# Optimization experiments

Hardware: AMD Instinct MI355X
Metric: run time of the kernel (lower is better)

Reference implementation:

```python
import jax, jax.numpy as jnp
import numpy as np

D = 4096          # input_dims
P = 1             # p in Get_Atten_map_mc
NUM_IMG = 16
N_PER = 64        # objects per image
R_PER = 512       # relations per image
LN_EPS = 1e-5


def _linear_params(key, out_dim, in_dim):
    kw, kb = jax.random.split(key)
    w = jax.random.normal(kw, (out_dim, in_dim), jnp.float32) * 0.02
    b = jax.random.normal(kb, (out_dim,), jnp.float32) * 0.02
    return w, b


def setup_inputs() -> dict:
    key = jax.random.key(0)
    ks = jax.random.split(key, 12)
    N = NUM_IMG * N_PER
    R = NUM_IMG * R_PER

    obj_feats = jax.random.normal(ks[0], (N, D), jnp.float32)
    phr_feats = jax.random.normal(ks[1], (R, D), jnp.float32)

    # im_inds: uniform N_PER objects per image
    im_inds = jnp.repeat(jnp.arange(NUM_IMG, dtype=jnp.int64), N_PER)

    # rel_inds: [img_idx, subj_global, obj_global], R_PER rels per image,
    # subject/object indices local-to-image then offset to global ids.
    subj_loc = jax.random.randint(ks[2], (NUM_IMG, R_PER), 0, N_PER)
    obj_loc = jax.random.randint(ks[3], (NUM_IMG, R_PER), 0, N_PER)
    offs = (jnp.arange(NUM_IMG) * N_PER)[:, None]
    img_col = jnp.repeat(jnp.arange(NUM_IMG), R_PER)
    rel_inds = jnp.stack(
        [img_col, (subj_loc + offs).reshape(-1), (obj_loc + offs).reshape(-1)], axis=1
    ).astype(jnp.int64)

    Ws_w, Ws_b = _linear_params(ks[4], D, D)       # ws
    Wo_w, Wo_b = _linear_params(ks[5], D, D)       # wo
    Ww_w, Ww_b = _linear_params(ks[6], P, D)       # w (attention logits)
    Wc_w, Wc_b = _linear_params(ks[7], D // 2, D)  # conv Linear
    Wt1_w, Wt1_b = _linear_params(ks[8], D // 4, D)
    Wt2_w, Wt2_b = _linear_params(ks[9], D, D // 4)
    ln_g = jnp.ones((D // 4,), jnp.float32)
    ln_b = jnp.zeros((D // 4,), jnp.float32)

    return {
        "obj_feats": obj_feats, "phr_feats": phr_feats,
        "im_inds": im_inds, "rel_inds": rel_inds, "num_img": NUM_IMG,
        "Ws_w": Ws_w, "Ws_b": Ws_b, "Wo_w": Wo_w, "Wo_b": Wo_b,
        "Ww_w": Ww_w, "Ww_b": Ww_b, "Wc_w": Wc_w, "Wc_b": Wc_b,
        "Wt1_w": Wt1_w, "Wt1_b": Wt1_b, "ln_g": ln_g, "ln_b": ln_b,
        "Wt2_w": Wt2_w, "Wt2_b": Wt2_b,
    }


def reference(obj_feats, phr_feats, im_inds, rel_inds, num_img,
              Ws_w, Ws_b, Wo_w, Wo_b, Ww_w, Ww_b, Wc_w, Wc_b,
              Wt1_w, Wt1_b, ln_g, ln_b, Wt2_w, Wt2_b):
    N, d = obj_feats.shape
    n_per = N // num_img
    R = rel_inds.shape[0]
    r_per = R // num_img
    p = Ww_w.shape[0]

    # ws/wo projections over all objects (original recomputes them per image
    # on the full obj_feats -- identical math, computed once here).
    ws_all = obj_feats @ Ws_w.T + Ws_b
    wo_all = obj_feats @ Wo_w.T + Wo_b

    subj = rel_inds[:, 1]
    objc = rel_inds[:, 2]
    prod = ws_all[subj] * wo_all[objc]               # [R, D]
    atten_f = (prod * phr_feats) @ Ww_w.T + Ww_b     # [R, p]

    # conv on object features
    conv_all = jax.nn.relu(obj_feats @ Wc_w.T + Wc_b)  # [N, D/2]

    subj_i = subj.reshape(num_img, r_per)
    objc_i = objc.reshape(num_img, r_per)
    af_i = atten_f.reshape(num_img, r_per, p)
    conv_i = conv_all.reshape(num_img, n_per, -1)

    self_mask = 1.0 - jnp.eye(n_per, dtype=jnp.float32)[:, :, None]  # [n,n,1]

    def per_image(s, o, af, conv_feats):
        head = jnp.minimum(s.min(), o.min())
        A = jnp.zeros((n_per, n_per, p), jnp.float32).at[s - head, o - head].add(af)
        A = jax.nn.sigmoid(A) * self_mask
        A = A / A.sum(1)                               # [n,n,p] / [n,p] (col-normalize)
        A2 = jnp.concatenate([A, A.transpose(1, 0, 2)], axis=-1)  # [n,n,2p]
        # mc_matmul: concat of per-channel mm -> channel-major reshape
        return jnp.einsum('ijc,jd->icd', A2, conv_feats).reshape(n_per, -1)

    ctx = jax.vmap(per_image)(subj_i, objc_i, af_i, conv_i)  # [num_img, n, 2p*D/2]
    ctx = ctx.reshape(N, -1)                                  # [N, D]

    # trans: Linear -> LayerNorm -> ReLU -> Linear
    h = ctx @ Wt1_w.T + Wt1_b
    mu = h.mean(-1, keepdims=True)
    var = ((h - mu) ** 2).mean(-1, keepdims=True)
    h = (h - mu) * jax.lax.rsqrt(var + LN_EPS) * ln_g + ln_b
    h = jax.nn.relu(h)
    out = h @ Wt2_w.T + Wt2_b

    return jax.nn.relu(obj_feats + out)
```

## Files before the change

### kernel.cpp

```cpp
#include <hip/hip_runtime.h>
#include <hip/hip_bf16.h>
#include <math.h>

#define D_   4096
#define NIMG 16
#define NPER 64
#define RPER 512
#define NTOT 1024
#define RTOT 8192
#define DC   2048
#define DT   1024
#define LDA  8192

typedef __attribute__((ext_vector_type(4))) float f32x4;
typedef __attribute__((ext_vector_type(8))) short bf16x8;

#define GLD16(gp, lp) __builtin_amdgcn_global_load_lds( \
    (const __attribute__((address_space(1))) unsigned int*)(gp), \
    (__attribute__((address_space(3))) unsigned int*)(lp), 16, 0, 0)

template<int N> __device__ __forceinline__ void waitvm() {
    asm volatile("s_waitcnt vmcnt(%0)" :: "n"(N) : "memory");
}

__device__ __forceinline__ void fma4(float4& d, float s, const float4 c) {
    d.x = fmaf(s, c.x, d.x); d.y = fmaf(s, c.y, d.y);
    d.z = fmaf(s, c.z, d.z); d.w = fmaf(s, c.w, d.w);
}
__device__ __forceinline__ void st4bf(__hip_bfloat16* p, float4 v) {
    union { __hip_bfloat16 h[4]; ushort4 u; } cv;
    cv.h[0] = __float2bfloat16(v.x); cv.h[1] = __float2bfloat16(v.y);
    cv.h[2] = __float2bfloat16(v.z); cv.h[3] = __float2bfloat16(v.w);
    *(ushort4*)p = cv.u;
}

__global__ __launch_bounds__(256) void cast_all(
    const float* __restrict__ obj, __hip_bfloat16* __restrict__ obj_bf,
    const float* __restrict__ Ws, const float* __restrict__ Wo,
    const float* __restrict__ Wc, __hip_bfloat16* __restrict__ wbuf,
    const float* __restrict__ b0, const float* __restrict__ b1,
    const float* __restrict__ b2, float* __restrict__ cb)
{
    const int b = blockIdx.x;
    if (b < 22528) {
        const float* s; __hip_bfloat16* d; int rb;
        if (b < 2048)       { s = obj; d = obj_bf;          rb = b; }
        else if (b < 10240) { s = Ws;  d = wbuf;            rb = b - 2048; }
        else if (b < 18432) { s = Wo;  d = wbuf + 16777216; rb = b - 10240; }
        else                { s = Wc;  d = wbuf + 33554432; rb = b - 18432; }
        const int i = (rb * 256 + threadIdx.x) * 8;
        float4 v0 = *(const float4*)(s + i);
        float4 v1 = *(const float4*)(s + i + 4);
        union { __hip_bfloat16 h[8]; ushort4 u[2]; } cv;
        cv.h[0] = __float2bfloat16(v0.x); cv.h[1] = __float2bfloat16(v0.y);
        cv.h[2] = __float2bfloat16(v0.z); cv.h[3] = __float2bfloat16(v0.w);
        cv.h[4] = __float2bfloat16(v1.x); cv.h[5] = __float2bfloat16(v1.y);
        cv.h[6] = __float2bfloat16(v1.z); cv.h[7] = __float2bfloat16(v1.w);
        *(ushort4*)(d + i)     = cv.u[0];
        *(ushort4*)(d + i + 4) = cv.u[1];
    } else {
        const int i = (b - 22528) * 256 + threadIdx.x;
        float v;
        if (i < 4096) v = b0[i];
        else if (i < 8192) v = b1[i - 4096];
        else v = b2[i - 8192];
        cb[i] = v;
    }
}

__global__ __launch_bounds__(256) void cast2(
    const float* __restrict__ Wt1, const float* __restrict__ Wt2,
    __hip_bfloat16* __restrict__ wt1r, __hip_bfloat16* __restrict__ wt2b)
{
    const int b = blockIdx.x;
    const int t = threadIdx.x;
    const float* s; __hip_bfloat16* d;
    if (b < 2048) {
        const int r = b, c = t * 8;
        s = Wt1 + (size_t)(r & 1023) * 4096 + (r >> 10) * 2048 + c;
        d = wt1r + (size_t)r * 2048 + c;
    } else {
        const int i = ((b - 2048) * 256 + t) * 8;
        s = Wt2 + i;
        d = wt2b + i;
    }
    float4 v0 = *(const float4*)s;
    float4 v1 = *(const float4*)(s + 4);
    union { __hip_bfloat16 h[8]; ushort4 u[2]; } cv;
    cv.h[0] = __float2bfloat16(v0.x); cv.h[1] = __float2bfloat16(v0.y);
    cv.h[2] = __float2bfloat16(v0.z); cv.h[3] = __float2bfloat16(v0.w);
    cv.h[4] = __float2bfloat16(v1.x); cv.h[5] = __float2bfloat16(v1.y);
    cv.h[6] = __float2bfloat16(v1.z); cv.h[7] = __float2bfloat16(v1.w);
    *(ushort4*)d       = cv.u[0];
    *(ushort4*)(d + 4) = cv.u[1];
}

template<int BM, int BN>
__global__ __launch_bounds__(256) void gemm_p2(
    const ushort* __restrict__ A, const ushort* __restrict__ B,
    const float* __restrict__ bias, const float* __restrict__ resid,
    float* __restrict__ C, __hip_bfloat16* __restrict__ C2,
    int M, int K, int ldc, int mode, int reluStart)
{
    constexpr int MREP = BM / 32;
    constexpr int NREP = BN / 32;
    constexpr int SLOTS = (BM + BN) * 4;
    constexpr int NPW = SLOTS / 256;
    constexpr int BUFE = SLOTS * 8;

    __shared__ ushort lds[3][BUFE];

    const int t = threadIdx.x;
    const int lane = t & 63;
    const int wid = t >> 6;
    const int wr = wid >> 1, wc = wid & 1;

    const int MT = M / BM;
    const int G = gridDim.x;
    const int bid = blockIdx.x;
    const int wgid = (bid & 7) * (G >> 3) + (bid >> 3);
    const int nt = wgid / MT, mt = wgid % MT;
    const int bm = mt * BM, bn = nt * BN;

    const ushort* gp[NPW];
    int loff[NPW];
#pragma unroll
    for (int i = 0; i < NPW; ++i) {
        const int slot = i * 256 + t;
        const bool isA = slot < BM * 4;
        const int s2 = isA ? slot : slot - BM * 4;
        const int row = s2 >> 2;
        const int q = (s2 & 3) ^ ((row >> 1) & 3);
        gp[i] = (isA ? A + (size_t)(bm + row) * K : B + (size_t)(bn + row) * K) + q * 8;
        loff[i] = slot * 8;
    }

    auto stage = [&](int b, int kpos) {
#pragma unroll
        for (int i = 0; i < NPW; ++i) GLD16(gp[i] + kpos, &lds[b][loff[i]]);
    };

    int aoff[MREP], boff[NREP];
    const int sx = (((lane >> 4) ^ ((lane >> 1) & 3))) << 3;
#pragma unroll
    for (int m = 0; m < MREP; ++m)
        aoff[m] = (wr * (BM / 2) + (lane & 15) + m * 16) * 32 + sx;
#pragma unroll
    for (int n = 0; n < NREP; ++n)
        boff[n] = BM * 32 + (wc * (BN / 2) + (lane & 15) + n * 16) * 32 + sx;

    f32x4 acc[MREP][NREP] = {};

    const int NT = K >> 5;
    stage(0, 0);
    stage(1, 32);
    if constexpr (NPW == 2) waitvm<2>();
    else if constexpr (NPW == 3) waitvm<3>();
    else waitvm<4>();
    __builtin_amdgcn_sched_barrier(0);
    __builtin_amdgcn_s_barrier();
    __builtin_amdgcn_sched_barrier(0);

    for (int tt = 0; tt < NT; ++tt) {
        const bool pf = (tt + 2 < NT);
        if (pf) stage((tt + 2) % 3, (tt + 2) << 5);
        __builtin_amdgcn_sched_barrier(0);

        const ushort* lb = lds[tt % 3];
        bf16x8 af[MREP], bfv[NREP];
#pragma unroll
        for (int m = 0; m < MREP; ++m) af[m] = *(const bf16x8*)(lb + aoff[m]);
#pragma unroll
        for (int n = 0; n < NREP; ++n) bfv[n] = *(const bf16x8*)(lb + boff[n]);
#pragma unroll
        for (int m = 0; m < MREP; ++m)
#pragma unroll
            for (int n = 0; n < NREP; ++n)
                acc[m][n] = __builtin_amdgcn_mfma_f32_16x16x32_bf16(
                    af[m], bfv[n], acc[m][n], 0, 0, 0);

        __builtin_amdgcn_sched_barrier(0);
        if (pf) {
            if constexpr (NPW == 2) waitvm<2>();
            else if constexpr (NPW == 3) waitvm<3>();
            else waitvm<4>();
        } else {
            waitvm<0>();
        }
        __builtin_amdgcn_sched_barrier(0);
        __builtin_amdgcn_s_barrier();
        __builtin_amdgcn_sched_barrier(0);
    }

    const int col0 = bn + wc * (BN / 2) + (lane & 15);
    const int row0 = bm + wr * (BM / 2) + ((lane >> 4) << 2);
#pragma unroll
    for (int m = 0; m < MREP; ++m) {
#pragma unroll
        for (int n = 0; n < NREP; ++n) {
            const int cn = col0 + n * 16;
            const float bz = bias ? bias[cn] : 0.f;
#pragma unroll
            for (int rg = 0; rg < 4; ++rg) {
                const int gm = row0 + m * 16 + rg;
                float v = acc[m][n][rg] + bz;
                if (mode == 2) {
                    v = fmaxf(v + resid[(size_t)gm * ldc + cn], 0.f);
                    C[(size_t)gm * ldc + cn] = v;
                } else if (mode == 4) {
                    if (cn < reluStart) {
                        C[(size_t)gm * ldc + cn] = v;
                    } else {
                        C2[(size_t)gm * 2048 + (cn - 8192)] =
                            __float2bfloat16(fmaxf(v, 0.f));
                    }
                } else {
                    C[(size_t)gm * ldc + cn] = v;
                }
            }
        }
    }
}

__global__ __launch_bounds__(256) void atten_kernel(
    const float* __restrict__ allout, const float* __restrict__ phr,
    const int* __restrict__ rel, const float* __restrict__ Www,
    const float* __restrict__ Wwb, float* __restrict__ atten)
{
    const int r = blockIdx.x;
    const int s = rel[r * 3 + 1], o = rel[r * 3 + 2];
    const int t = threadIdx.x;
    const float4* pws = (const float4*)(allout + (size_t)s * LDA);
    const float4* pwo = (const float4*)(allout + (size_t)o * LDA + 4096);
    const float4* pph = (const float4*)(phr + (size_t)r * D_);
    const float4* pww = (const float4*)Www;
    float sum = 0.f;
    for (int qq = t; qq < D_ / 4; qq += 256) {
        float4 a = pws[qq], b = pwo[qq], c = pph[qq], w = pww[qq];
        sum += a.x * b.x * c.x * w.x + a.y * b.y * c.y * w.y
             + a.z * b.z * c.z * w.z + a.w * b.w * c.w * w.w;
    }
    for (int off = 32; off > 0; off >>= 1) sum += __shfl_down(sum, off);
    __shared__ float red[4];
    if ((t & 63) == 0) red[t >> 6] = sum;
    __syncthreads();
    if (t == 0) atten[r] = red[0] + red[1] + red[2] + red[3] + Wwb[0];
}

__global__ __launch_bounds__(256) void build_A(
    const int* __restrict__ rel, const float* __restrict__ atten,
    float* __restrict__ Anorm)
{
    const int g = blockIdx.x;
    const int t = threadIdx.x;
    __shared__ float Am[64][64];
    __shared__ float S[64];
    __shared__ int headSh;
    for (int i = t; i < 4096; i += 256) ((float*)Am)[i] = 0.f;
    if (t == 0) headSh = 0x7fffffff;

    int lmin = 0x7fffffff;
    for (int rr = t; rr < RPER; rr += 256) {
        const int base = (g * RPER + rr) * 3;
        lmin = min(lmin, min(rel[base + 1], rel[base + 2]));
    }
    for (int off = 32; off > 0; off >>= 1) lmin = min(lmin, __shfl_down(lmin, off));
    __syncthreads();
    if ((t & 63) == 0) atomicMin(&headSh, lmin);
    __syncthreads();
    const int head = headSh;

    for (int rr = t; rr < RPER; rr += 256) {
        const int base = (g * RPER + rr) * 3;
        atomicAdd(&Am[rel[base + 1] - head][rel[base + 2] - head],
                  atten[g * RPER + rr]);
    }
    __syncthreads();

    for (int idx = t; idx < 4096; idx += 256) {
        const int i = idx >> 6, j = idx & 63;
        float v = 1.f / (1.f + expf(-Am[i][j]));
        if (i == j) v = 0.f;
        Am[i][j] = v;
    }
    __syncthreads();

    if (t < 64) {
        float sum = 0.f;
        for (int k = 0; k < 64; ++k) sum += Am[t][k];
        S[t] = sum;
    }
    __syncthreads();

    float* outg = Anorm + (size_t)g * 4096;
    for (int idx = t; idx < 4096; idx += 256) {
        const int j = idx & 63;
        outg[idx] = ((const float*)Am)[idx] / S[j];
    }
}

__global__ __launch_bounds__(256) void amult_ln(
    const float* __restrict__ Anorm, const float* __restrict__ P,
    const float* __restrict__ w1b, const float* __restrict__ gamma,
    const float* __restrict__ beta, __hip_bfloat16* __restrict__ hb)
{
    const int g = blockIdx.x >> 6;
    const int i = blockIdx.x & 63;
    const int t = threadIdx.x;
    __shared__ float Ar[64], Ac[64];
    if (t < 64) Ar[t] = Anorm[(size_t)g * 4096 + i * 64 + t];
    else if (t < 128) { const int j = t - 64; Ac[j] = Anorm[(size_t)g * 4096 + j * 64 + i]; }
    __syncthreads();

    const float* pg = P + (size_t)g * 64 * 2048;
    float4 v = {0, 0, 0, 0};
    for (int j = 0; j < 64; ++j) {
        float4 p1 = *(const float4*)(pg + (size_t)j * 2048 + (t << 2));
        float4 p2 = *(const float4*)(pg + (size_t)j * 2048 + 1024 + (t << 2));
        fma4(v, Ar[j], p1);
        fma4(v, Ac[j], p2);
    }
    float4 b0 = *(const float4*)(w1b + (t << 2));
    v.x += b0.x; v.y += b0.y; v.z += b0.z; v.w += b0.w;

    float s  = v.x + v.y + v.z + v.w;
    float ss = v.x * v.x + v.y * v.y + v.z * v.z + v.w * v.w;
    for (int off = 32; off > 0; off >>= 1) {
        s  += __shfl_down(s, off);
        ss += __shfl_down(ss, off);
    }
    __shared__ float rs[4], rss[4];
    if ((t & 63) == 0) { rs[t >> 6] = s; rss[t >> 6] = ss; }
    __syncthreads();
    const float tot  = rs[0] + rs[1] + rs[2] + rs[3];
    const float tot2 = rss[0] + rss[1] + rss[2] + rss[3];
    const float mu   = tot * (1.f / DT);
    const float var  = tot2 * (1.f / DT) - mu * mu;
    const float rstd = rsqrtf(var + 1e-5f);
    float4 g4 = *(const float4*)(gamma + (t << 2));
    float4 b4 = *(const float4*)(beta + (t << 2));
    float4 o;
    o.x = fmaxf(fmaf((v.x - mu) * rstd, g4.x, b4.x), 0.f);
    o.y = fmaxf(fmaf((v.y - mu) * rstd, g4.y, b4.y), 0.f);
    o.z = fmaxf(fmaf((v.z - mu) * rstd, g4.z, b4.z), 0.f);
    o.w = fmaxf(fmaf((v.w - mu) * rstd, g4.w, b4.w), 0.f);
    st4bf(hb + (size_t)(g * 64 + i) * DT + (t << 2), o);
}

extern "C" void kernel_launch(void* const* d_in, const int* in_sizes, int n_in,
                              void* d_out, int out_size, void* d_ws, size_t ws_size,
                              hipStream_t stream)
{
    const float* obj   = (const float*)d_in[0];
    const float* phr   = (const float*)d_in[1];
    const int*   rel   = (const int*)d_in[3];
    const float* Ws_w  = (const float*)d_in[5];
    const float* Ws_b  = (const float*)d_in[6];
    const float* Wo_w  = (const float*)d_in[7];
    const float* Wo_b  = (const float*)d_in[8];
    const float* Ww_w  = (const float*)d_in[9];
    const float* Ww_b  = (const float*)d_in[10];
    const float* Wc_w  = (const float*)d_in[11];
    const float* Wc_b  = (const float*)d_in[12];
    const float* Wt1_w = (const float*)d_in[13];
    const float* Wt1_b = (const float*)d_in[14];
    const float* ln_g  = (const float*)d_in[15];
    const float* ln_b  = (const float*)d_in[16];
    const float* Wt2_w = (const float*)d_in[17];
    const float* Wt2_b = (const float*)d_in[18];
    float* out = (float*)d_out;

    float* ws = (float*)d_ws;
    __hip_bfloat16* wbuf   = (__hip_bfloat16*)ws;
    __hip_bfloat16* wt1r   = (__hip_bfloat16*)ws;
    __hip_bfloat16* wt2b   = (__hip_bfloat16*)(ws + 2097152);
    __hip_bfloat16* obj_bf = (__hip_bfloat16*)(ws + 20971520);
    float* allout = ws + 23068672;
    float* Pbuf   = allout;
    __hip_bfloat16* h_bf = (__hip_bfloat16*)(allout + 2097152);
    __hip_bfloat16* conv_bf = (__hip_bfloat16*)(ws + 31457280);
    float* atten  = ws + 32505856;
    float* Anorm  = ws + 32514048;
    float* cbias  = ws + 32579584;

    const dim3 blk(256);

    cast_all<<<dim3(22568), blk, 0, stream>>>(
        obj, obj_bf, Ws_w, Wo_w, Wc_w, wbuf, Ws_b, Wo_b, Wc_b, cbias);

    gemm_p2<128, 128><<<dim3(640), blk, 0, stream>>>(
        (const ushort*)obj_bf, (const ushort*)wbuf, cbias, nullptr,
        allout, conv_bf, NTOT, D_, LDA, 4, 8192);

    cast2<<<dim3(4096), blk, 0, stream>>>(Wt1_w, Wt2_w, wt1r, wt2b);

    atten_kernel<<<dim3(RTOT), blk, 0, stream>>>(allout, phr, rel, Ww_w, Ww_b, atten);
    build_A<<<dim3(NIMG), blk, 0, stream>>>(rel, atten, Anorm);

    gemm_p2<64, 64><<<dim3(512), blk, 0, stream>>>(
        (const ushort*)conv_bf, (const ushort*)wt1r, nullptr, nullptr,
        Pbuf, nullptr, NTOT, DC, DC, 0, 0);

    amult_ln<<<dim3(1024), blk, 0, stream>>>(Anorm, Pbuf, Wt1_b, ln_g, ln_b, h_bf);

    gemm_p2<128, 128><<<dim3(256), blk, 0, stream>>>(
        (const ushort*)h_bf, (const ushort*)wt2b, Wt2_b, obj,
        out, nullptr, NTOT, DT, D_, 2, 0);
}
```

Measured before the change: 318.0 us.

## Store Ws/Wo projections as bf16, merge weight casts, retile final GEMM

The first GEMM now writes the Ws/Wo projection outputs as bf16 instead of fp32, and the attention kernel reads these bf16 rows with 16-byte loads, roughly halving the gather traffic. The Wt1/Wt2 cast kernel is folded into the main cast kernel so one launch handles every weight conversion, with the workspace layout rearranged so the buffers no longer alias. The final GEMM switches from 128x128 to 64x128 tiles with twice as many blocks for better occupancy. Storing the projections in bf16 loses precision in the attention logits.

```diff
diff --git a/kernel.cpp b/kernel.cpp
--- a/kernel.cpp
+++ b/kernel.cpp
@@ -10,7 +10,7 @@
 #define RTOT 8192
 #define DC   2048
 #define DT   1024
-#define LDA  8192
+#define LDW  8192
 
 typedef __attribute__((ext_vector_type(4))) float f32x4;
 typedef __attribute__((ext_vector_type(8))) short bf16x8;
@@ -33,66 +33,49 @@
     cv.h[2] = __float2bfloat16(v.z); cv.h[3] = __float2bfloat16(v.w);
     *(ushort4*)p = cv.u;
 }
+__device__ __forceinline__ float bf2f(ushort u) {
+    union { float f; unsigned int i; } c; c.i = (unsigned int)u << 16; return c.f;
+}
 
 __global__ __launch_bounds__(256) void cast_all(
     const float* __restrict__ obj, __hip_bfloat16* __restrict__ obj_bf,
     const float* __restrict__ Ws, const float* __restrict__ Wo,
     const float* __restrict__ Wc, __hip_bfloat16* __restrict__ wbuf,
+    const float* __restrict__ Wt1, __hip_bfloat16* __restrict__ wt1r,
+    const float* __restrict__ Wt2, __hip_bfloat16* __restrict__ wt2b,
     const float* __restrict__ b0, const float* __restrict__ b1,
     const float* __restrict__ b2, float* __restrict__ cb)
 {
     const int b = blockIdx.x;
-    if (b < 22528) {
-        const float* s; __hip_bfloat16* d; int rb;
-        if (b < 2048)       { s = obj; d = obj_bf;          rb = b; }
-        else if (b < 10240) { s = Ws;  d = wbuf;            rb = b - 2048; }
-        else if (b < 18432) { s = Wo;  d = wbuf + 16777216; rb = b - 10240; }
-        else                { s = Wc;  d = wbuf + 33554432; rb = b - 18432; }
-        const int i = (rb * 256 + threadIdx.x) * 8;
-        float4 v0 = *(const float4*)(s + i);
-        float4 v1 = *(const float4*)(s + i + 4);
-        union { __hip_bfloat16 h[8]; ushort4 u[2]; } cv;
-        cv.h[0] = __float2bfloat16(v0.x); cv.h[1] = __float2bfloat16(v0.y);
-        cv.h[2] = __float2bfloat16(v0.z); cv.h[3] = __float2bfloat16(v0.w);
-        cv.h[4] = __float2bfloat16(v1.x); cv.h[5] = __float2bfloat16(v1.y);
-        cv.h[6] = __float2bfloat16(v1.z); cv.h[7] = __float2bfloat16(v1.w);
-        *(ushort4*)(d + i)     = cv.u[0];
-        *(ushort4*)(d + i + 4) = cv.u[1];
-    } else {
-        const int i = (b - 22528) * 256 + threadIdx.x;
+    const int t = threadIdx.x;
+    if (b >= 26624) {
+        const int i = (b - 26624) * 256 + t;
         float v;
         if (i < 4096) v = b0[i];
         else if (i < 8192) v = b1[i - 4096];
         else v = b2[i - 8192];
         cb[i] = v;
-    }
-}
-
-__global__ __launch_bounds__(256) void cast2(
-    const float* __restrict__ Wt1, const float* __restrict__ Wt2,
-    __hip_bfloat16* __restrict__ wt1r, __hip_bfloat16* __restrict__ wt2b)
-{
-    const int b = blockIdx.x;
-    const int t = threadIdx.x;
+        return;
+    }
     const float* s; __hip_bfloat16* d;
-    if (b < 2048) {
-        const int r = b, c = t * 8;
-        s = Wt1 + (size_t)(r & 1023) * 4096 + (r >> 10) * 2048 + c;
-        d = wt1r + (size_t)r * 2048 + c;
-    } else {
-        const int i = ((b - 2048) * 256 + t) * 8;
-        s = Wt2 + i;
-        d = wt2b + i;
-    }
-    float4 v0 = *(const float4*)s;
-    float4 v1 = *(const float4*)(s + 4);
+    if (b < 2048)       { s = obj + (size_t)b * 2048;            d = obj_bf + (size_t)b * 2048; }
+    else if (b < 10240) { const int rb = b - 2048;  s = Ws + (size_t)rb * 2048; d = wbuf + (size_t)rb * 2048; }
+    else if (b < 18432) { const int rb = b - 10240; s = Wo + (size_t)rb * 2048; d = wbuf + 16777216 + (size_t)rb * 2048; }
+    else if (b < 22528) { const int rb = b - 18432; s = Wc + (size_t)rb * 2048; d = wbuf + 33554432 + (size_t)rb * 2048; }
+    else if (b < 24576) { const int r = b - 22528;
+                          s = Wt1 + (size_t)(r & 1023) * 4096 + (r >> 10) * 2048;
+                          d = wt1r + (size_t)r * 2048; }
+    else                { const int rb = b - 24576; s = Wt2 + (size_t)rb * 2048; d = wt2b + (size_t)rb * 2048; }
+    const int i = t * 8;
+    float4 v0 = *(const float4*)(s + i);
+    float4 v1 = *(const float4*)(s + i + 4);
     union { __hip_bfloat16 h[8]; ushort4 u[2]; } cv;
     cv.h[0] = __float2bfloat16(v0.x); cv.h[1] = __float2bfloat16(v0.y);
     cv.h[2] = __float2bfloat16(v0.z); cv.h[3] = __float2bfloat16(v0.w);
     cv.h[4] = __float2bfloat16(v1.x); cv.h[5] = __float2bfloat16(v1.y);
     cv.h[6] = __float2bfloat16(v1.z); cv.h[7] = __float2bfloat16(v1.w);
-    *(ushort4*)d       = cv.u[0];
-    *(ushort4*)(d + 4) = cv.u[1];
+    *(ushort4*)(d + i)     = cv.u[0];
+    *(ushort4*)(d + i + 4) = cv.u[1];
 }
 
 template<int BM, int BN>
@@ -100,7 +83,8 @@
     const ushort* __restrict__ A, const ushort* __restrict__ B,
     const float* __restrict__ bias, const float* __restrict__ resid,
     float* __restrict__ C, __hip_bfloat16* __restrict__ C2,
-    int M, int K, int ldc, int mode, int reluStart)
+    __hip_bfloat16* __restrict__ C3,
+    int M, int K, int ldc, int mode)
 {
     constexpr int MREP = BM / 32;
     constexpr int NREP = BN / 32;
@@ -205,15 +189,13 @@
                 const int gm = row0 + m * 16 + rg;
                 float v = acc[m][n][rg] + bz;
                 if (mode == 2) {
-                    v = fmaxf(v + resid[(size_t)gm * ldc + cn], 0.f);
-                    C[(size_t)gm * ldc + cn] = v;
+                    C[(size_t)gm * ldc + cn] = fmaxf(v + resid[(size_t)gm * ldc + cn], 0.f);
                 } else if (mode == 4) {
-                    if (cn < reluStart) {
-                        C[(size_t)gm * ldc + cn] = v;
-                    } else {
-                        C2[(size_t)gm * 2048 + (cn - 8192)] =
+                    if (cn < 8192)
+                        C2[(size_t)gm * LDW + cn] = __float2bfloat16(v);
+                    else
+                        C3[(size_t)gm * 2048 + (cn - 8192)] =
                             __float2bfloat16(fmaxf(v, 0.f));
-                    }
                 } else {
                     C[(size_t)gm * ldc + cn] = v;
                 }
@@ -223,22 +205,36 @@
 }
 
 __global__ __launch_bounds__(256) void atten_kernel(
-    const float* __restrict__ allout, const float* __restrict__ phr,
+    const ushort* __restrict__ wswo, const float* __restrict__ phr,
     const int* __restrict__ rel, const float* __restrict__ Www,
     const float* __restrict__ Wwb, float* __restrict__ atten)
 {
     const int r = blockIdx.x;
     const int s = rel[r * 3 + 1], o = rel[r * 3 + 2];
     const int t = threadIdx.x;
-    const float4* pws = (const float4*)(allout + (size_t)s * LDA);
-    const float4* pwo = (const float4*)(allout + (size_t)o * LDA + 4096);
-    const float4* pph = (const float4*)(phr + (size_t)r * D_);
-    const float4* pww = (const float4*)Www;
+    const ushort* pws = wswo + (size_t)s * LDW;
+    const ushort* pwo = wswo + (size_t)o * LDW + 4096;
+    const float*  pph = phr + (size_t)r * D_;
     float sum = 0.f;
-    for (int qq = t; qq < D_ / 4; qq += 256) {
-        float4 a = pws[qq], b = pwo[qq], c = pph[qq], w = pww[qq];
-        sum += a.x * b.x * c.x * w.x + a.y * b.y * c.y * w.y
-             + a.z * b.z * c.z * w.z + a.w * b.w * c.w * w.w;
+#pragma unroll
+    for (int half = 0; half < 2; ++half) {
+        const int q = t * 8 + half * 2048;
+        ushort4 w0 = *(const ushort4*)(pws + q);
+        ushort4 w1 = *(const ushort4*)(pws + q + 4);
+        ushort4 u0 = *(const ushort4*)(pwo + q);
+        ushort4 u1 = *(const ushort4*)(pwo + q + 4);
+        float4 p0 = *(const float4*)(pph + q);
+        float4 p1 = *(const float4*)(pph + q + 4);
+        float4 g0 = *(const float4*)(Www + q);
+        float4 g1 = *(const float4*)(Www + q + 4);
+        sum += bf2f(w0.x) * bf2f(u0.x) * p0.x * g0.x
+             + bf2f(w0.y) * bf2f(u0.y) * p0.y * g0.y
+             + bf2f(w0.z) * bf2f(u0.z) * p0.z * g0.z
+             + bf2f(w0.w) * bf2f(u0.w) * p0.w * g0.w
+             + bf2f(w1.x) * bf2f(u1.x) * p1.x * g1.x
+             + bf2f(w1.y) * bf2f(u1.y) * p1.y * g1.y
+             + bf2f(w1.z) * bf2f(u1.z) * p1.z * g1.z
+             + bf2f(w1.w) * bf2f(u1.w) * p1.w * g1.w;
     }
     for (int off = 32; off > 0; off >>= 1) sum += __shfl_down(sum, off);
     __shared__ float red[4];
@@ -371,39 +367,39 @@
     float* out = (float*)d_out;
 
     float* ws = (float*)d_ws;
-    __hip_bfloat16* wbuf   = (__hip_bfloat16*)ws;
-    __hip_bfloat16* wt1r   = (__hip_bfloat16*)ws;
-    __hip_bfloat16* wt2b   = (__hip_bfloat16*)(ws + 2097152);
-    __hip_bfloat16* obj_bf = (__hip_bfloat16*)(ws + 20971520);
-    float* allout = ws + 23068672;
-    float* Pbuf   = allout;
-    __hip_bfloat16* h_bf = (__hip_bfloat16*)(allout + 2097152);
-    __hip_bfloat16* conv_bf = (__hip_bfloat16*)(ws + 31457280);
+    __hip_bfloat16* wbuf    = (__hip_bfloat16*)ws;
+    __hip_bfloat16* h_bf    = (__hip_bfloat16*)ws;
+    __hip_bfloat16* obj_bf  = (__hip_bfloat16*)(ws + 20971520);
+    float* Pbuf             = ws + 20971520;
+    __hip_bfloat16* wswo_bf = (__hip_bfloat16*)(ws + 23068672);
+    __hip_bfloat16* conv_bf = (__hip_bfloat16*)(ws + 27262976);
+    __hip_bfloat16* wt1r    = (__hip_bfloat16*)(ws + 28311552);
+    __hip_bfloat16* wt2b    = (__hip_bfloat16*)(ws + 30408704);
     float* atten  = ws + 32505856;
     float* Anorm  = ws + 32514048;
     float* cbias  = ws + 32579584;
 
     const dim3 blk(256);
 
-    cast_all<<<dim3(22568), blk, 0, stream>>>(
-        obj, obj_bf, Ws_w, Wo_w, Wc_w, wbuf, Ws_b, Wo_b, Wc_b, cbias);
+    cast_all<<<dim3(26664), blk, 0, stream>>>(
+        obj, obj_bf, Ws_w, Wo_w, Wc_w, wbuf, Wt1_w, wt1r, Wt2_w, wt2b,
+        Ws_b, Wo_b, Wc_b, cbias);
 
     gemm_p2<128, 128><<<dim3(640), blk, 0, stream>>>(
         (const ushort*)obj_bf, (const ushort*)wbuf, cbias, nullptr,
-        allout, conv_bf, NTOT, D_, LDA, 4, 8192);
-
-    cast2<<<dim3(4096), blk, 0, stream>>>(Wt1_w, Wt2_w, wt1r, wt2b);
-
-    atten_kernel<<<dim3(RTOT), blk, 0, stream>>>(allout, phr, rel, Ww_w, Ww_b, atten);
+        nullptr, wswo_bf, conv_bf, NTOT, D_, 0, 4);
+
+    atten_kernel<<<dim3(RTOT), blk, 0, stream>>>(
+        (const ushort*)wswo_bf, phr, rel, Ww_w, Ww_b, atten);
     build_A<<<dim3(NIMG), blk, 0, stream>>>(rel, atten, Anorm);
 
     gemm_p2<64, 64><<<dim3(512), blk, 0, stream>>>(
         (const ushort*)conv_bf, (const ushort*)wt1r, nullptr, nullptr,
-        Pbuf, nullptr, NTOT, DC, DC, 0, 0);
+        Pbuf, nullptr, nullptr, NTOT, DC, DC, 0);
 
     amult_ln<<<dim3(1024), blk, 0, stream>>>(Anorm, Pbuf, Wt1_b, ln_g, ln_b, h_bf);
 
-    gemm_p2<128, 128><<<dim3(256), blk, 0, stream>>>(
+    gemm_p2<64, 128><<<dim3(512), blk, 0, stream>>>(
         (const ushort*)h_bf, (const ushort*)wt2b, Wt2_b, obj,
-        out, nullptr, NTOT, DT, D_, 2, 0);
-}
+        out, nullptr, nullptr, NTOT, DT, D_, 2);
+}
```

After: 299.1 us. 5.9% less time.
